# Kernel tuning notes

Hardware: AMD Instinct MI355X
Metric: run time of the kernel (lower is better)

## Reference

```python
import jax, jax.numpy as jnp
import numpy as np
import math

BS, S, D, H = 16, 512, 1024, 16
DK = D // H
HALF = H // 2
R, GAMMA, EPS = 1.0, 0.1, 1e-6


def _alibi(n_heads, maxpos):
    # n_heads=16 is a power of 2
    start = 2.0 ** (-2.0 ** (-(math.log2(n_heads) - 3)))
    slopes = np.array([start * start ** i for i in range(n_heads)], dtype=np.float32) * -1.0
    pos = np.arange(maxpos)
    rel = np.abs(pos[None, :] - pos[:, None]).astype(np.float32)
    return jnp.asarray((slopes[:, None, None] * rel)[None])  # (1,H,maxpos,maxpos)


def setup_inputs() -> dict:
    key = jax.random.key(0)
    ks = jax.random.split(key, 6)
    sc = 1.0 / math.sqrt(D)
    x = jax.random.normal(ks[0], (BS, S, D), dtype=jnp.float32)
    Wq = jax.random.normal(ks[1], (D, D), dtype=jnp.float32) * sc
    Wk = jax.random.normal(ks[2], (D, D), dtype=jnp.float32) * sc
    Wv = jax.random.normal(ks[3], (D, D), dtype=jnp.float32) * sc
    Wo = jax.random.normal(ks[4], (D, D), dtype=jnp.float32) * sc
    bq = jnp.zeros((D,), jnp.float32)
    bk = jnp.zeros((D,), jnp.float32)
    bv = jnp.zeros((D,), jnp.float32)
    bo = jnp.zeros((D,), jnp.float32)
    alibi = _alibi(H, S)  # pre-sliced to seq_len (original slices [:,:,:S,:S])
    # src_mask for mask=0: np.triu(ones,k=0)==0 -> strictly lower triangular
    mask = jnp.tril(jnp.ones((S, S), dtype=bool), k=-1)[None, None]
    return {"x": x, "Wq": Wq, "bq": bq, "Wk": Wk, "bk": bk, "Wv": Wv,
            "bv": bv, "Wo": Wo, "bo": bo, "alibi": alibi, "mask": mask}


def _map_psi(x, r):
    x_y = jax.nn.sigmoid(x[..., -1])           # (b,h,s)
    return x[..., :-1] * x_y[..., None] * r, x_y * r


def _penumbral(q, k, r=R, gamma=GAMMA, eps=EPS):
    q_x, q_y = _map_psi(q, r)
    k_x, k_y = _map_psi(k, r)
    q_y = q_y[..., :, None]                    # (b,h,s,1)
    k_y = k_y[..., None, :]                    # (b,h,1,s)
    x_q_y = jnp.sqrt(r ** 2 - q_y ** 2 + eps)
    x_k_y = jnp.sqrt(r ** 2 - k_y ** 2 + eps)
    # euclidean cdist over last dim (d_k-1)
    qn = jnp.sum(q_x ** 2, axis=-1)[..., :, None]
    kn = jnp.sum(k_x ** 2, axis=-1)[..., None, :]
    d2 = qn + kn - 2.0 * jnp.einsum('bhqd,bhkd->bhqk', q_x, k_x)
    pd = jnp.sqrt(jnp.maximum(d2, 0.0) + 1e-12)
    lca = jnp.maximum(jnp.maximum(q_y ** 2, k_y ** 2),
                      r ** 2 - ((x_q_y + x_k_y - pd) / 2.0) ** 2)
    lca_out = ((pd ** 2 + k_y ** 2 - q_y ** 2) / (2.0 * pd + eps)) ** 2 + q_y ** 2
    exists = (pd <= x_q_y) | ((pd - x_q_y) ** 2 + k_y ** 2 <= r ** 2)
    return -gamma * jnp.where(exists, lca, lca_out)


def _masked_softmax_zeropad(scores, mask):
    scores = jnp.where(mask, scores, -1e32)
    p = jax.nn.softmax(scores, axis=-1)
    return p.at[:, :, 0, :].set(0.0)  # zero_pad=True (mask==0 branch)


def reference(x, Wq, bq, Wk, bk, Wv, bv, Wo, bo, alibi, mask):
    bs, s, d = x.shape
    q = (x @ Wq.T + bq).reshape(bs, s, H, DK).transpose(0, 2, 1, 3)
    k = (x @ Wk.T + bk).reshape(bs, s, H, DK).transpose(0, 2, 1, 3)
    v = (x @ Wv.T + bv).reshape(bs, s, H, DK).transpose(0, 2, 1, 3)
    inv = 1.0 / math.sqrt(DK)
    # first half heads: standard dot-product attention + alibi
    sc1 = jnp.einsum('bhqd,bhkd->bhqk', q[:, :HALF], k[:, :HALF]) * inv
    sc1 = sc1 + alibi[:, :HALF, :s, :s]
    p1 = _masked_softmax_zeropad(sc1, mask)
    o1 = jnp.einsum('bhqk,bhkd->bhqd', p1, v[:, :HALF])
    # second half heads: penumbral hyperbolic score + alibi
    sc2 = _penumbral(q[:, HALF:], k[:, HALF:]) * inv
    sc2 = sc2 + alibi[:, HALF:, :s, :s]
    p2 = _masked_softmax_zeropad(sc2, mask)
    o2 = jnp.einsum('bhqk,bhkd->bhqd', p2, v[:, HALF:])
    out = jnp.concatenate([o1, o2], axis=1)  # (b,H,s,dk)
    out = out.transpose(0, 2, 1, 3).reshape(bs, s, d)
    return out @ Wo.T + bo
```

## Files before the change

kernel.cpp:

```cpp
#include <hip/hip_runtime.h>
#include <math.h>

#define BS 16
#define S 512
#define D 1024
#define H 16
#define DK 64
#define HALF 8

typedef __attribute__((ext_vector_type(8))) short short8v;
typedef __attribute__((ext_vector_type(4))) float f32x4;
typedef unsigned short ushort_t;

#define L2E 1.4426950408889634f
#define SC_STD (0.125f * L2E)
#define SC_PEN (-0.0125f * L2E)

__device__ __forceinline__ ushort_t f2bf(float f) {
  union { float f; unsigned u; } v; v.f = f;
  unsigned r = v.u + 0x7fffu + ((v.u >> 16) & 1u);
  return (ushort_t)(r >> 16);
}
__device__ __forceinline__ unsigned packbf(float a, float b) {
  return (unsigned)f2bf(a) | ((unsigned)f2bf(b) << 16);
}
__device__ __forceinline__ float bf2f(ushort_t u) {
  union { unsigned u; float f; } v; v.u = ((unsigned)u) << 16;
  return v.f;
}
__device__ __forceinline__ unsigned cvtpk(float lo, float hi) {
  unsigned r;
  asm("v_cvt_pk_bf16_f32 %0, %1, %2" : "=v"(r) : "v"(lo), "v"(hi));
  return r;
}

__device__ __forceinline__ void gload16(const void* g, void* l) {
  __builtin_amdgcn_global_load_lds(
      (const __attribute__((address_space(1))) unsigned int*)g,
      (__attribute__((address_space(3))) unsigned int*)l, 16, 0, 0);
}

__global__ __launch_bounds__(256) void cvt_fused(
    const float* __restrict__ x, const float* __restrict__ Wq,
    const float* __restrict__ Wk, const float* __restrict__ Wv,
    const float* __restrict__ Wo, ushort_t* __restrict__ dst) {
  const int bid = blockIdx.x;
  const float* src;
  int si;
  if (bid < 4096) {
    src = x; si = bid * 256 + threadIdx.x;
  } else {
    const int k = bid - 4096;
    const int w = k >> 9;
    src = (w == 0) ? Wq : (w == 1) ? Wk : (w == 2) ? Wv : Wo;
    si = (k & 511) * 256 + threadIdx.x;
  }
  const int di = bid * 256 + threadIdx.x;
  const float4 a = *(const float4*)(src + (size_t)si * 8);
  const float4 b = *(const float4*)(src + (size_t)si * 8 + 4);
  union { short8v v; unsigned u[4]; } t;
  t.u[0] = packbf(a.x, a.y);
  t.u[1] = packbf(a.z, a.w);
  t.u[2] = packbf(b.x, b.y);
  t.u[3] = packbf(b.z, b.w);
  *(short8v*)(dst + (size_t)di * 8) = t.v;
}

__global__ __launch_bounds__(256) void gemm_qkv(
    const ushort_t* __restrict__ A, const ushort_t* __restrict__ Wcat,
    const float* __restrict__ bq, const float* __restrict__ bk,
    const float* __restrict__ bv, ushort_t* __restrict__ QK,
    ushort_t* __restrict__ Vt) {
  const int tid = threadIdx.x;
  const int lane = tid & 63, wid = tid >> 6;
  const int wr = wid >> 1, wc = wid & 1;
  const int lq = lane & 15, g = lane >> 4;
  const int bn = blockIdx.x;
  const int bm = blockIdx.y;
  const int mat = bn >> 3;

  __shared__ __align__(16) ushort_t sA[128 * 64];
  __shared__ __align__(16) ushort_t sB[128 * 64];

  f32x4 acc[4][4];
#pragma unroll
  for (int i = 0; i < 4; i++)
#pragma unroll
    for (int j = 0; j < 4; j++) acc[i][j] = (f32x4){0.f, 0.f, 0.f, 0.f};

  for (int k0 = 0; k0 < 1024; k0 += 64) {
#pragma unroll
    for (int is = 0; is < 4; ++is) {
      const int gi = is * 256 + tid;
      const int row = gi >> 3, slot = gi & 7;
      const int sslot = slot ^ (row & 7);
      gload16(A + (size_t)(bm * 128 + row) * 1024 + k0 + sslot * 8,
              &sA[(is * 256 + wid * 64) * 8]);
      gload16(Wcat + (size_t)(bn * 128 + row) * 1024 + k0 + sslot * 8,
              &sB[(is * 256 + wid * 64) * 8]);
    }
    __syncthreads();
#pragma unroll
    for (int ks = 0; ks < 2; ++ks) {
      short8v af[4], bf[4];
#pragma unroll
      for (int i = 0; i < 4; ++i) {
        const int arow = wr * 64 + i * 16 + lq;
        af[i] = *(const short8v*)&sA[arow * 64 + (((ks * 4 + g) ^ (arow & 7)) * 8)];
        const int brow = wc * 64 + i * 16 + lq;
        bf[i] = *(const short8v*)&sB[brow * 64 + (((ks * 4 + g) ^ (brow & 7)) * 8)];
      }
#pragma unroll
      for (int i = 0; i < 4; ++i)
#pragma unroll
        for (int j = 0; j < 4; ++j)
          acc[i][j] =
              __builtin_amdgcn_mfma_f32_16x16x32_bf16(af[i], bf[j], acc[i][j], 0, 0, 0);
    }
    __syncthreads();
  }

  const float* bias = (mat == 0) ? bq : (mat == 1) ? bk : bv;
  const size_t NQKV = (size_t)BS * H * S * DK;
#pragma unroll
  for (int j = 0; j < 4; ++j) {
    const int n = ((bn & 7) * 128) + wc * 64 + j * 16 + lq;
    const float bvv = bias[n];
#pragma unroll
    for (int i = 0; i < 4; ++i) {
      const int mb = bm * 128 + wr * 64 + i * 16 + g * 4;
      if (mat < 2) {
        ushort_t* C = QK + (size_t)mat * NQKV;
#pragma unroll
        for (int r = 0; r < 4; ++r) {
          const int m = mb + r;
          C[((((size_t)(m >> 9) * H + (n >> 6)) * S + (m & 511)) * DK) +
            (n & 63)] = f2bf(acc[i][j][r] + bvv);
        }
      } else {
        const int bb = mb >> 9, s0 = mb & 511;
        uint2 u;
        u.x = packbf(acc[i][j][0] + bvv, acc[i][j][1] + bvv);
        u.y = packbf(acc[i][j][2] + bvv, acc[i][j][3] + bvv);
        *(uint2*)(Vt + (((size_t)bb * H + (n >> 6)) * DK + (n & 63)) * S + s0) = u;
      }
    }
  }
}

__global__ __launch_bounds__(256) void gemm_out(
    const ushort_t* __restrict__ A, const ushort_t* __restrict__ B,
    const float* __restrict__ bias, float* __restrict__ C) {
  const int tid = threadIdx.x;
  const int lane = tid & 63, wid = tid >> 6;
  const int wr = wid >> 1, wc = wid & 1;
  const int lq = lane & 15, g = lane >> 4;
  const int bn = blockIdx.x;
  const int bm = blockIdx.y;

  __shared__ __align__(16) ushort_t sA[128 * 64];
  __shared__ __align__(16) ushort_t sB[128 * 64];

  f32x4 acc[4][4];
#pragma unroll
  for (int i = 0; i < 4; i++)
#pragma unroll
    for (int j = 0; j < 4; j++) acc[i][j] = (f32x4){0.f, 0.f, 0.f, 0.f};

  for (int k0 = 0; k0 < 1024; k0 += 64) {
#pragma unroll
    for (int is = 0; is < 4; ++is) {
      const int gi = is * 256 + tid;
      const int row = gi >> 3, slot = gi & 7;
      const int sslot = slot ^ (row & 7);
      gload16(A + (size_t)(bm * 128 + row) * 1024 + k0 + sslot * 8,
              &sA[(is * 256 + wid * 64) * 8]);
      gload16(B + (size_t)(bn * 128 + row) * 1024 + k0 + sslot * 8,
              &sB[(is * 256 + wid * 64) * 8]);
    }
    __syncthreads();
#pragma unroll
    for (int ks = 0; ks < 2; ++ks) {
      short8v af[4], bf[4];
#pragma unroll
      for (int i = 0; i < 4; ++i) {
        const int arow = wr * 64 + i * 16 + lq;
        af[i] = *(const short8v*)&sA[arow * 64 + (((ks * 4 + g) ^ (arow & 7)) * 8)];
        const int brow = wc * 64 + i * 16 + lq;
        bf[i] = *(const short8v*)&sB[brow * 64 + (((ks * 4 + g) ^ (brow & 7)) * 8)];
      }
#pragma unroll
      for (int i = 0; i < 4; ++i)
#pragma unroll
        for (int j = 0; j < 4; ++j)
          acc[i][j] =
              __builtin_amdgcn_mfma_f32_16x16x32_bf16(af[i], bf[j], acc[i][j], 0, 0, 0);
    }
    __syncthreads();
  }

#pragma unroll
  for (int j = 0; j < 4; ++j) {
    const int n = bn * 128 + wc * 64 + j * 16 + lq;
    const float bvv = bias[n];
#pragma unroll
    for (int i = 0; i < 4; ++i) {
      const int mb = bm * 128 + wr * 64 + i * 16 + g * 4;
#pragma unroll
      for (int r = 0; r < 4; ++r)
        C[(size_t)(mb + r) * 1024 + n] = acc[i][j][r] + bvv;
    }
  }
}

__global__ __launch_bounds__(256) void psi_kernel(
    ushort_t* __restrict__ Q, ushort_t* __restrict__ K,
    float4* __restrict__ QPn, float4* __restrict__ KPn) {
  const int s = blockIdx.x * 4 + (threadIdx.x >> 6);
  const int yy = blockIdx.y, b = blockIdx.z;
  const int isK = yy >> 3, hh = yy & 7;
  ushort_t* X = isK ? K : Q;
  float4* Pn = isK ? KPn : QPn;
  const int h = HALF + hh;
  ushort_t* row = X + (((size_t)b * H + h) * S + s) * DK;
  const int t = threadIdx.x & 63;
  const float v = bf2f(row[t]);
  const float last = __shfl(v, 63, 64);
  const float y = 1.0f / (1.0f + expf(-last));
  const float xv = (t < 63) ? v * y : y;
  const ushort_t bvv = f2bf(xv);
  row[t] = bvv;
  const float xr = bf2f(bvv);
  float sq = (t < 63) ? xr * xr : 0.0f;
#pragma unroll
  for (int off = 32; off; off >>= 1) sq += __shfl_xor(sq, off, 64);
  if (t == 0)
    Pn[((size_t)b * HALF + hh) * S + s] =
        make_float4(sq, y * y, sqrtf(1.0f - y * y + 1e-6f), 0.0f);
}

template <bool MASK>
__device__ __forceinline__ void attn_tile(
    const char* sKb, const char* sVb, const float4* sPn, const short8v* qf,
    float qn, float qy2, float xqy, bool pen, float slopeL, int qg, int kt0,
    int lq, int g, f32x4* o, float& m, float& lacc) {
  float p[4][4];
  float tmax = -1e30f;
#pragma unroll
  for (int t4 = 0; t4 < 4; ++t4) {
    f32x4 acc = (f32x4){0.f, 0.f, 0.f, 0.f};
    const int row = t4 * 16 + lq;
#pragma unroll
    for (int c = 0; c < 2; ++c) {
      const short8v ka =
          *(const short8v*)(sKb + row * 128 + (((c * 4 + g) ^ (row & 7)) * 16));
      acc = __builtin_amdgcn_mfma_f32_16x16x32_bf16(ka, qf[c], acc, 0, 0, 0);
    }
#pragma unroll
    for (int r = 0; r < 4; ++r) {
      const int kg = kt0 + t4 * 16 + g * 4 + r;
      const float abL = slopeL * (float)(qg - kg);
      float s;
      if (!pen) {
        s = acc[r] * SC_STD + abL;
      } else {
        const float4 kp = sPn[t4 * 16 + g * 4 + r];
        const float kn = kp.x, ky2 = kp.y, xky = kp.z;
        const float d2 = qn + kn - 2.0f * acc[r];
        const float tt = fmaxf(d2, 0.0f) + 1e-12f;
        const float rs = rsqrtf(tt);
        const float pd = tt * rs;
        const float tmp = (xqy + xky - pd) * 0.5f;
        const float lca = fmaxf(fmaxf(qy2, ky2), 1.0f - tmp * tmp);
        const float num = (d2 + ky2 - qy2) * (0.5f * rs);
        const float lout = num * num + qy2;
        const float dxy = pd - xqy;
        const bool ex = (pd <= xqy) || (dxy * dxy + ky2 <= 1.0f);
        s = (ex ? lca : lout) * SC_PEN + abL;
      }
      if (MASK && kg >= qg) s = -1e30f;
      p[t4][r] = s;
      tmax = fmaxf(tmax, s);
    }
  }
  tmax = fmaxf(tmax, __shfl_xor(tmax, 16, 64));
  tmax = fmaxf(tmax, __shfl_xor(tmax, 32, 64));
  const float mnew = fmaxf(m, tmax);
  if (__any(mnew > m)) {
    const float fsc = exp2f(m - mnew);
#pragma unroll
    for (int dt = 0; dt < 4; ++dt) o[dt] *= fsc;
    lacc *= fsc;
    m = mnew;
  }
  float ls = 0.f;
#pragma unroll
  for (int t4 = 0; t4 < 4; ++t4)
#pragma unroll
    for (int r = 0; r < 4; ++r) {
      float pv = exp2f(p[t4][r] - m);
      if (MASK && p[t4][r] < -1e29f) pv = 0.f;
      p[t4][r] = pv;
      ls += pv;
    }
  ls += __shfl_xor(ls, 16, 64);
  ls += __shfl_xor(ls, 32, 64);
  lacc += ls;

  unsigned pk0[4], pk1[4];
#pragma unroll
  for (int t4 = 0; t4 < 4; ++t4) {
    pk0[t4] = cvtpk(p[t4][0], p[t4][1]);
    pk1[t4] = cvtpk(p[t4][2], p[t4][3]);
  }
  const int s0 = lq | (((g * 2) & 3) << 4);
  const int s1 = lq | (((g * 2 + 1) & 3) << 4);
  const bool hi = (g >= 2);
#pragma unroll
  for (int c = 0; c < 2; ++c) {
    const unsigned a0 = (unsigned)__shfl((int)pk0[2 * c], s0, 64);
    const unsigned b0 = (unsigned)__shfl((int)pk0[2 * c + 1], s0, 64);
    const unsigned a1 = (unsigned)__shfl((int)pk1[2 * c], s0, 64);
    const unsigned b1 = (unsigned)__shfl((int)pk1[2 * c + 1], s0, 64);
    const unsigned a2 = (unsigned)__shfl((int)pk0[2 * c], s1, 64);
    const unsigned b2 = (unsigned)__shfl((int)pk0[2 * c + 1], s1, 64);
    const unsigned a3 = (unsigned)__shfl((int)pk1[2 * c], s1, 64);
    const unsigned b3 = (unsigned)__shfl((int)pk1[2 * c + 1], s1, 64);
    union { short8v v; unsigned u[4]; } pb;
    pb.u[0] = hi ? b0 : a0;
    pb.u[1] = hi ? b1 : a1;
    pb.u[2] = hi ? b2 : a2;
    pb.u[3] = hi ? b3 : a3;
#pragma unroll
    for (int dt = 0; dt < 4; ++dt) {
      const int vr = dt * 16 + lq;
      const short8v va =
          *(const short8v*)(sVb + vr * 128 + (((c * 4 + g) ^ (vr & 7)) * 16));
      o[dt] = __builtin_amdgcn_mfma_f32_16x16x32_bf16(va, pb.v, o[dt], 0, 0, 0);
    }
  }
}

__global__ __launch_bounds__(256, 4) void attn_mfma(
    const ushort_t* __restrict__ Qf, const ushort_t* __restrict__ Kf,
    const ushort_t* __restrict__ Vt, const float4* __restrict__ QPn,
    const float4* __restrict__ KPn, ushort_t* __restrict__ O) {
  const int dsp = blockIdx.x;
  const int xcd = dsp & 7, idx = dsp >> 3;
  const int bh = xcd * 32 + (idx & 31);
  const int qb = 7 - (idx >> 5);
  const int b = bh >> 4, h = bh & 15;
  const int tid = threadIdx.x, lane = tid & 63, wid = tid >> 6;
  const int lq = lane & 15, g = lane >> 4;
  const bool pen = (h >= HALF);
  const float slopeL = -exp2f(-0.5f * (float)(h + 1)) * L2E;
  const size_t hoff = ((size_t)b * H + h) * S * DK;
  const ushort_t* Vslab = Vt + hoff;
  const size_t bhh = (size_t)b * HALF + (h & (HALF - 1));

  __shared__ __align__(16) char sK[2][8192];
  __shared__ __align__(16) char sV[2][8192];
  __shared__ __align__(16) float4 sPen[2][64];

  const int qg = qb * 64 + wid * 16 + lq;

  short8v qf[2];
  {
    const ushort_t* qr = Qf + hoff + (size_t)qg * DK;
    qf[0] = *(const short8v*)(qr + g * 8);
    qf[1] = *(const short8v*)(qr + 32 + g * 8);
    if (pen && g == 3) qf[1][7] = 0;
  }
  float qn = 0, qy2 = 0, xqy = 0;
  if (pen) {
    const float4 a = QPn[bhh * S + qg];
    qn = a.x; qy2 = a.y; xqy = a.z;
  }

  const int r8 = lane >> 3;
  const int sl = ((lane & 7) ^ r8) * 8;

  auto stage = [&](int buf, int kt) {
#pragma unroll
    for (int i = 0; i < 2; ++i) {
      const int row = wid * 16 + i * 8 + r8;
      gload16(Kf + hoff + (size_t)(kt * 64 + row) * DK + sl,
              &sK[buf][(wid * 2 + i) * 1024]);
      gload16(Vslab + (size_t)row * S + kt * 64 + sl,
              &sV[buf][(wid * 2 + i) * 1024]);
    }
    if (pen && wid == 0)
      gload16(&KPn[bhh * S + kt * 64 + lane], &sPen[buf][0]);
  };

  f32x4 o[4];
#pragma unroll
  for (int dt = 0; dt < 4; ++dt) o[dt] = (f32x4){0.f, 0.f, 0.f, 0.f};
  float m = -1e30f, l = 0.f;

  stage(0, qb);
  __syncthreads();
  int cur = 0;
  for (int kt = qb; kt >= 0; --kt) {
    if (kt > 0) stage(cur ^ 1, kt - 1);
    if (kt == qb)
      attn_tile<true>(sK[cur], sV[cur], sPen[cur], qf, qn, qy2, xqy, pen,
                      slopeL, qg, kt * 64, lq, g, o, m, l);
    else
      attn_tile<false>(sK[cur], sV[cur], sPen[cur], qf, qn, qy2, xqy, pen,
                       slopeL, qg, kt * 64, lq, g, o, m, l);
    __syncthreads();
    cur ^= 1;
  }

  const float invl = (qg == 0) ? 0.f : 1.0f / l;
  ushort_t* orow = O + ((size_t)b * S + qg) * D + h * DK;
#pragma unroll
  for (int dt = 0; dt < 4; ++dt) {
    uint2 u;
    u.x = cvtpk(o[dt][0] * invl, o[dt][1] * invl);
    u.y = cvtpk(o[dt][2] * invl, o[dt][3] * invl);
    *(uint2*)(orow + dt * 16 + g * 4) = u;
  }
}

extern "C" void kernel_launch(void* const* d_in, const int* in_sizes, int n_in,
                              void* d_out, int out_size, void* d_ws,
                              size_t ws_size, hipStream_t stream) {
  (void)in_sizes; (void)n_in; (void)out_size; (void)ws_size;
  const float* x  = (const float*)d_in[0];
  const float* Wq = (const float*)d_in[1];
  const float* bq = (const float*)d_in[2];
  const float* Wk = (const float*)d_in[3];
  const float* bk = (const float*)d_in[4];
  const float* Wv = (const float*)d_in[5];
  const float* bv = (const float*)d_in[6];
  const float* Wo = (const float*)d_in[7];
  const float* bo = (const float*)d_in[8];
  float* out = (float*)d_out;

  const size_t NQKV = (size_t)BS * H * S * DK;
  const size_t NW = (size_t)D * D;
  ushort_t* ws  = (ushort_t*)d_ws;
  ushort_t* Qb  = ws;
  ushort_t* Kbb = Qb + NQKV;
  ushort_t* Vtb = Kbb + NQKV;
  ushort_t* Ob  = Vtb + NQKV;
  ushort_t* xb  = Ob + NQKV;
  ushort_t* Wqb = xb + NQKV;
  ushort_t* Wkb = Wqb + NW;
  ushort_t* Wvb = Wkb + NW;
  ushort_t* Wob = Wvb + NW;
  float4* QPn = (float4*)(Wob + NW);
  float4* KPn = QPn + (size_t)BS * HALF * S;

  cvt_fused<<<dim3(4096 + 4 * 512), 256, 0, stream>>>(x, Wq, Wk, Wv, Wo, xb);
  gemm_qkv<<<dim3(24, 64), 256, 0, stream>>>(xb, Wqb, bq, bk, bv, Qb, Vtb);
  psi_kernel<<<dim3(S / 4, 16, BS), 256, 0, stream>>>(Qb, Kbb, QPn, KPn);
  attn_mfma<<<dim3(2048), 256, 0, stream>>>(Qb, Kbb, Vtb, QPn, KPn, Ob);
  gemm_out<<<dim3(8, 64), 256, 0, stream>>>(Ob, Wob, bo, out);
}
```

Before: 171.6 us.

## Double-buffer LDS in projection GEMMs and remap blocks per XCD

Both the QKV and output projection GEMMs now keep two LDS buffers. The next K-tile's global-to-LDS loads are issued before the MFMA work on the current tile, so load latency overlaps with compute and one barrier per iteration is removed. The launch grids are flattened to 1D, and the QKV grid is remapped so each XCD handles a contiguous group of N-tiles for better L2 locality. The QKV epilogue also converts accumulator pairs with a packed bf16 conversion helper. In exchange, LDS use per block doubles, which can lower occupancy.

```diff
diff --git a/kernel.cpp b/kernel.cpp
--- a/kernel.cpp
+++ b/kernel.cpp
@@ -71,16 +71,18 @@
     const float* __restrict__ bq, const float* __restrict__ bk,
     const float* __restrict__ bv, ushort_t* __restrict__ QK,
     ushort_t* __restrict__ Vt) {
+  const int id = blockIdx.x;
+  const int xcd = id & 7, r0 = id >> 3;
+  const int bn = xcd * 3 + (r0 % 3);
+  const int bm = r0 / 3;
   const int tid = threadIdx.x;
   const int lane = tid & 63, wid = tid >> 6;
   const int wr = wid >> 1, wc = wid & 1;
   const int lq = lane & 15, g = lane >> 4;
-  const int bn = blockIdx.x;
-  const int bm = blockIdx.y;
   const int mat = bn >> 3;
 
-  __shared__ __align__(16) ushort_t sA[128 * 64];
-  __shared__ __align__(16) ushort_t sB[128 * 64];
+  __shared__ __align__(16) ushort_t sA[2][128 * 64];
+  __shared__ __align__(16) ushort_t sB[2][128 * 64];
 
   f32x4 acc[4][4];
 #pragma unroll
@@ -88,27 +90,35 @@
 #pragma unroll
     for (int j = 0; j < 4; j++) acc[i][j] = (f32x4){0.f, 0.f, 0.f, 0.f};
 
-  for (int k0 = 0; k0 < 1024; k0 += 64) {
+  const int grow = (tid * 8 + 0) >> 3;
+  auto stage = [&](int buf, int k0) {
 #pragma unroll
     for (int is = 0; is < 4; ++is) {
       const int gi = is * 256 + tid;
       const int row = gi >> 3, slot = gi & 7;
       const int sslot = slot ^ (row & 7);
       gload16(A + (size_t)(bm * 128 + row) * 1024 + k0 + sslot * 8,
-              &sA[(is * 256 + wid * 64) * 8]);
+              &sA[buf][(is * 256 + wid * 64) * 8]);
       gload16(Wcat + (size_t)(bn * 128 + row) * 1024 + k0 + sslot * 8,
-              &sB[(is * 256 + wid * 64) * 8]);
-    }
-    __syncthreads();
+              &sB[buf][(is * 256 + wid * 64) * 8]);
+    }
+  };
+  (void)grow;
+
+  stage(0, 0);
+  __syncthreads();
+  for (int t = 0; t < 16; ++t) {
+    if (t < 15) stage((t + 1) & 1, (t + 1) * 64);
+    const int buf = t & 1;
 #pragma unroll
     for (int ks = 0; ks < 2; ++ks) {
       short8v af[4], bf[4];
 #pragma unroll
       for (int i = 0; i < 4; ++i) {
         const int arow = wr * 64 + i * 16 + lq;
-        af[i] = *(const short8v*)&sA[arow * 64 + (((ks * 4 + g) ^ (arow & 7)) * 8)];
+        af[i] = *(const short8v*)&sA[buf][arow * 64 + (((ks * 4 + g) ^ (arow & 7)) * 8)];
         const int brow = wc * 64 + i * 16 + lq;
-        bf[i] = *(const short8v*)&sB[brow * 64 + (((ks * 4 + g) ^ (brow & 7)) * 8)];
+        bf[i] = *(const short8v*)&sB[buf][brow * 64 + (((ks * 4 + g) ^ (brow & 7)) * 8)];
       }
 #pragma unroll
       for (int i = 0; i < 4; ++i)
@@ -129,19 +139,21 @@
 #pragma unroll
     for (int i = 0; i < 4; ++i) {
       const int mb = bm * 128 + wr * 64 + i * 16 + g * 4;
+      const unsigned p0 = cvtpk(acc[i][j][0] + bvv, acc[i][j][1] + bvv);
+      const unsigned p1 = cvtpk(acc[i][j][2] + bvv, acc[i][j][3] + bvv);
       if (mat < 2) {
-        ushort_t* C = QK + (size_t)mat * NQKV;
-#pragma unroll
-        for (int r = 0; r < 4; ++r) {
-          const int m = mb + r;
-          C[((((size_t)(m >> 9) * H + (n >> 6)) * S + (m & 511)) * DK) +
-            (n & 63)] = f2bf(acc[i][j][r] + bvv);
-        }
+        ushort_t* base = QK + (size_t)mat * NQKV +
+                         ((((size_t)(mb >> 9) * H + (n >> 6)) * S + (mb & 511)) * DK) +
+                         (n & 63);
+        base[0] = (ushort_t)p0;
+        base[DK] = (ushort_t)(p0 >> 16);
+        base[2 * DK] = (ushort_t)p1;
+        base[3 * DK] = (ushort_t)(p1 >> 16);
       } else {
         const int bb = mb >> 9, s0 = mb & 511;
         uint2 u;
-        u.x = packbf(acc[i][j][0] + bvv, acc[i][j][1] + bvv);
-        u.y = packbf(acc[i][j][2] + bvv, acc[i][j][3] + bvv);
+        u.x = p0;
+        u.y = p1;
         *(uint2*)(Vt + (((size_t)bb * H + (n >> 6)) * DK + (n & 63)) * S + s0) = u;
       }
     }
@@ -151,15 +163,15 @@
 __global__ __launch_bounds__(256) void gemm_out(
     const ushort_t* __restrict__ A, const ushort_t* __restrict__ B,
     const float* __restrict__ bias, float* __restrict__ C) {
+  const int id = blockIdx.x;
+  const int bn = id & 7, bm = id >> 3;
   const int tid = threadIdx.x;
   const int lane = tid & 63, wid = tid >> 6;
   const int wr = wid >> 1, wc = wid & 1;
   const int lq = lane & 15, g = lane >> 4;
-  const int bn = blockIdx.x;
-  const int bm = blockIdx.y;
-
-  __shared__ __align__(16) ushort_t sA[128 * 64];
-  __shared__ __align__(16) ushort_t sB[128 * 64];
+
+  __shared__ __align__(16) ushort_t sA[2][128 * 64];
+  __shared__ __align__(16) ushort_t sB[2][128 * 64];
 
   f32x4 acc[4][4];
 #pragma unroll
@@ -167,27 +179,33 @@
 #pragma unroll
     for (int j = 0; j < 4; j++) acc[i][j] = (f32x4){0.f, 0.f, 0.f, 0.f};
 
-  for (int k0 = 0; k0 < 1024; k0 += 64) {
+  auto stage = [&](int buf, int k0) {
 #pragma unroll
     for (int is = 0; is < 4; ++is) {
       const int gi = is * 256 + tid;
       const int row = gi >> 3, slot = gi & 7;
       const int sslot = slot ^ (row & 7);
       gload16(A + (size_t)(bm * 128 + row) * 1024 + k0 + sslot * 8,
-              &sA[(is * 256 + wid * 64) * 8]);
+              &sA[buf][(is * 256 + wid * 64) * 8]);
       gload16(B + (size_t)(bn * 128 + row) * 1024 + k0 + sslot * 8,
-              &sB[(is * 256 + wid * 64) * 8]);
-    }
-    __syncthreads();
+              &sB[buf][(is * 256 + wid * 64) * 8]);
+    }
+  };
+
+  stage(0, 0);
+  __syncthreads();
+  for (int t = 0; t < 16; ++t) {
+    if (t < 15) stage((t + 1) & 1, (t + 1) * 64);
+    const int buf = t & 1;
 #pragma unroll
     for (int ks = 0; ks < 2; ++ks) {
       short8v af[4], bf[4];
 #pragma unroll
       for (int i = 0; i < 4; ++i) {
         const int arow = wr * 64 + i * 16 + lq;
-        af[i] = *(const short8v*)&sA[arow * 64 + (((ks * 4 + g) ^ (arow & 7)) * 8)];
+        af[i] = *(const short8v*)&sA[buf][arow * 64 + (((ks * 4 + g) ^ (arow & 7)) * 8)];
         const int brow = wc * 64 + i * 16 + lq;
-        bf[i] = *(const short8v*)&sB[brow * 64 + (((ks * 4 + g) ^ (brow & 7)) * 8)];
+        bf[i] = *(const short8v*)&sB[buf][brow * 64 + (((ks * 4 + g) ^ (brow & 7)) * 8)];
       }
 #pragma unroll
       for (int i = 0; i < 4; ++i)
@@ -455,8 +473,8 @@
   float4* KPn = QPn + (size_t)BS * HALF * S;
 
   cvt_fused<<<dim3(4096 + 4 * 512), 256, 0, stream>>>(x, Wq, Wk, Wv, Wo, xb);
-  gemm_qkv<<<dim3(24, 64), 256, 0, stream>>>(xb, Wqb, bq, bk, bv, Qb, Vtb);
+  gemm_qkv<<<dim3(1536), 256, 0, stream>>>(xb, Wqb, bq, bk, bv, Qb, Vtb);
   psi_kernel<<<dim3(S / 4, 16, BS), 256, 0, stream>>>(Qb, Kbb, QPn, KPn);
   attn_mfma<<<dim3(2048), 256, 0, stream>>>(Qb, Kbb, Vtb, QPn, KPn, Ob);
-  gemm_out<<<dim3(8, 64), 256, 0, stream>>>(Ob, Wob, bo, out);
-}
+  gemm_out<<<dim3(512), 256, 0, stream>>>(Ob, Wob, bo, out);
+}
```

After: 173.8 us. About the same (+1.3%).
